# Optimization experiments

Measured on AMD Instinct MI355X. Metric: run time of the kernel, lower is better.

## Reference

```python
import jax, jax.numpy as jnp
import numpy as np

HIDDEN = 2048
HEAD = 256
VDIM = 512  # double_v_dim=True -> 2*head_size
GAMMA = 0.96875
SCALE_BASE = 512.0  # xpos default


def _rotate_every_two(x):
    # (x0, x1, x2, x3, ...) -> (-x1, x0, -x3, x2, ...)
    x1 = x[..., ::2]
    x2 = x[..., 1::2]
    return jnp.stack((-x2, x1), axis=-1).reshape(x.shape)


def _xpos(x, downscale=False, offset=0):
    # Standard XPOS (rotary + exponential scaling) as used in RetNet repos.
    S, d = x.shape[1], x.shape[2]
    d2 = d // 2
    scale_vec = (jnp.arange(0, d, 2, dtype=jnp.float32) + 0.4 * d) / (1.4 * d)  # [d2]
    pos = jnp.arange(S + offset, dtype=jnp.float32)
    scale = scale_vec[None, :] ** (pos[:, None] / SCALE_BASE)  # [S+off, d2]
    inv_freq = 1.0 / (10000.0 ** (jnp.arange(d2, dtype=jnp.float32) / d2))
    sinusoid = pos[:, None] * inv_freq[None, :]  # [S+off, d2]
    sin, cos = jnp.sin(sinusoid), jnp.cos(sinusoid)
    scale, sin, cos = scale[-S:], sin[-S:], cos[-S:]
    if downscale:
        scale = 1.0 / scale
    sin_s = jnp.repeat(sin * scale, 2, axis=-1)  # duplicate_interleave -> [S, d]
    cos_s = jnp.repeat(cos * scale, 2, axis=-1)
    return x * cos_s[None] + _rotate_every_two(x) * sin_s[None]


def _decay_matrix(S):
    # D[n, m] = gamma^(n-m) for n >= m else 0 (NaN/overflow-safe)
    n = jnp.arange(S, dtype=jnp.float32)
    diff = n[:, None] - n[None, :]
    mask = diff >= 0
    return jnp.where(mask, GAMMA ** jnp.where(mask, diff, 0.0), 0.0)


def setup_inputs() -> dict:
    key = jax.random.key(0)
    k1, k2, k3, k4 = jax.random.split(key, 4)
    B, S = 4, 4096
    X = jax.random.normal(k1, (B, S, HIDDEN), dtype=jnp.float32)
    W_Q = jax.random.normal(k2, (HIDDEN, HEAD), dtype=jnp.float32) / HIDDEN
    W_K = jax.random.normal(k3, (HIDDEN, HEAD), dtype=jnp.float32) / HIDDEN
    W_V = jax.random.normal(k4, (HIDDEN, VDIM), dtype=jnp.float32) / HIDDEN
    return {"X": X, "W_Q": W_Q, "W_K": W_K, "W_V": W_V}


def reference(X, W_Q, W_K, W_V):
    S = X.shape[1]
    Q = _xpos(X @ W_Q)                      # [B, S, HEAD]
    K = _xpos(X @ W_K, downscale=True)      # [B, S, HEAD]
    V = X @ W_V                             # [B, S, VDIM]
    D = _decay_matrix(S)                    # [S, S]
    retention = jnp.einsum('bqd,bkd->bqk', Q, K) * D[None]  # [B, S, S]
    return retention @ V                    # [B, S, VDIM]
```

## Files before the change

### kernel.cpp

```cpp
#include <hip/hip_runtime.h>
#include <math.h>

#define NB 4
#define SEQ 4096
#define HID 2048
#define DH 256
#define DV 512
#define NQKV 1024
#define CHUNK 128
#define NCH 32
#define MROWS (NB * SEQ)
#define GAMMA 0.96875f
#define GAMMA_INV 1.0322580645161290f
#define LOG2_GAMMA (-0.045803689613124794f)
#define LOG2_10000 13.287712379549449f

typedef __attribute__((ext_vector_type(8))) short short8;
typedef __attribute__((ext_vector_type(4))) float floatx4;

__device__ __forceinline__ unsigned short bf16_rne(float v) {
    unsigned int u = __float_as_uint(v);
    u += 0x7fff + ((u >> 16) & 1);
    return (unsigned short)(u >> 16);
}
__device__ __forceinline__ float b2f(unsigned short h) {
    return __uint_as_float((unsigned int)h << 16);
}

__device__ __forceinline__ void gld16(const void* g, void* l) {
    __builtin_amdgcn_global_load_lds(
        reinterpret_cast<const __attribute__((address_space(1))) unsigned int*>(
            reinterpret_cast<uintptr_t>(g)),
        reinterpret_cast<__attribute__((address_space(3))) unsigned int*>(
            reinterpret_cast<uintptr_t>(l)),
        16, 0, 0);
}

__global__ __launch_bounds__(256) void xcvt_kernel(
    const float* __restrict__ X, unsigned short* __restrict__ Xb)
{
    const int i = blockIdx.x * 256 + threadIdx.x;
    float4 x = ((const float4*)X)[i];
    ushort4 h;
    h.x = bf16_rne(x.x); h.y = bf16_rne(x.y);
    h.z = bf16_rne(x.z); h.w = bf16_rne(x.w);
    ((ushort4*)Xb)[i] = h;
}

__global__ __launch_bounds__(256) void wcvt_kernel(
    const float* __restrict__ WQ, const float* __restrict__ WK,
    const float* __restrict__ WV, unsigned short* __restrict__ Bt)
{
    __shared__ unsigned short sh[64][65];
    const int bid = blockIdx.x;
    const int kt = bid & 31;
    const int ntile = bid >> 5;
    const int k0 = kt * 64, n0 = ntile * 64;

    const float* W; int ld, nl0;
    if (n0 < 256)      { W = WQ; ld = DH; nl0 = n0; }
    else if (n0 < 512) { W = WK; ld = DH; nl0 = n0 - 256; }
    else               { W = WV; ld = DV; nl0 = n0 - 512; }

    const int t = threadIdx.x;
#pragma unroll
    for (int p = 0; p < 4; p++) {
        const int kl = (t >> 4) + p * 16;
        const int ng = (t & 15) * 4;
        float4 w = *(const float4*)&W[(size_t)(k0 + kl) * ld + nl0 + ng];
        sh[kl][ng + 0] = bf16_rne(w.x);
        sh[kl][ng + 1] = bf16_rne(w.y);
        sh[kl][ng + 2] = bf16_rne(w.z);
        sh[kl][ng + 3] = bf16_rne(w.w);
    }
    __syncthreads();
#pragma unroll
    for (int p = 0; p < 4; p++) {
        const int nl = (t >> 4) + p * 16;
        const int kg = (t & 15) * 4;
        ushort4 h;
        h.x = sh[kg + 0][nl]; h.y = sh[kg + 1][nl];
        h.z = sh[kg + 2][nl]; h.w = sh[kg + 3][nl];
        *(ushort4*)&Bt[(size_t)(n0 + nl) * HID + k0 + kg] = h;
    }
}

__global__ __launch_bounds__(256, 2) void qkv_mfma_kernel(
    const unsigned short* __restrict__ Xb, const unsigned short* __restrict__ Bt,
    unsigned short* __restrict__ Qb, unsigned short* __restrict__ Kb,
    unsigned short* __restrict__ Kt, unsigned short* __restrict__ Vt)
{
    __shared__ unsigned short Ah[2 * 128 * 32];
    __shared__ unsigned short Bh[2 * 128 * 32];

    const int bid = blockIdx.x;
    const int xcd = bid & 7;
    const int nt  = (bid >> 3) & 7;
    const int mt  = (xcd << 4) | (bid >> 6);
    const int m0 = mt * 128, n0 = nt * 128;

    const int t = threadIdx.x;
    const int w = t >> 6, lane = t & 63;
    const int wm = (w & 1) << 6;
    const int wn = (w >> 1) << 6;

    floatx4 acc[4][4];
#pragma unroll
    for (int i = 0; i < 4; i++)
#pragma unroll
        for (int j = 0; j < 4; j++) acc[i][j] = (floatx4)0.0f;

    const int srow = lane >> 2, scol = (lane & 3) * 8;
    const size_t aoff = (size_t)(m0 + w * 32 + srow) * HID + scol;
    const size_t boff = (size_t)(n0 + w * 32 + srow) * HID + scol;

    const int fr = lane & 15, fq = (lane >> 4) * 8;

    for (int k0 = 0; k0 < HID; k0 += 64) {
        __syncthreads();
#pragma unroll
        for (int s = 0; s < 2; s++)
#pragma unroll
            for (int q = 0; q < 2; q++) {
                gld16(Xb + aoff + (size_t)q * 16 * HID + k0 + s * 32,
                      &Ah[s * 4096 + (w * 32 + q * 16) * 32]);
                gld16(Bt + boff + (size_t)q * 16 * HID + k0 + s * 32,
                      &Bh[s * 4096 + (w * 32 + q * 16) * 32]);
            }
        __syncthreads();

#pragma nounroll
        for (int s = 0; s < 2; s++) {
            short8 ah[4], bh[4];
#pragma unroll
            for (int i = 0; i < 4; i++)
                ah[i] = *(const short8*)&Ah[s * 4096 + (wm + i * 16 + fr) * 32 + fq];
#pragma unroll
            for (int j = 0; j < 4; j++)
                bh[j] = *(const short8*)&Bh[s * 4096 + (wn + j * 16 + fr) * 32 + fq];
#pragma unroll
            for (int i = 0; i < 4; i++)
#pragma unroll
                for (int j = 0; j < 4; j++)
                    acc[i][j] = __builtin_amdgcn_mfma_f32_16x16x32_bf16(ah[i], bh[j], acc[i][j], 0, 0, 0);
        }
    }

    const int cl = lane & 15, rq = (lane >> 4) << 2;
    if (n0 >= 512) {
#pragma unroll
        for (int i = 0; i < 4; i++)
#pragma unroll
            for (int j = 0; j < 4; j++) {
                const int c = n0 - 512 + wn + j * 16 + cl;
#pragma unroll
                for (int r = 0; r < 4; r++) {
                    const int m = m0 + wm + i * 16 + rq + r;
                    Vt[(size_t)c * MROWS + m] = bf16_rne(acc[i][j][r]);
                }
            }
    } else {
        const bool isQ = (n0 < 256);
        unsigned short* dst = isQ ? Qb : Kb;
        const float sgn = isQ ? 1.f : -1.f;
        const int nb = isQ ? n0 : n0 - 256;
#pragma unroll
        for (int j = 0; j < 4; j++) {
            const int c = nb + wn + j * 16 + cl;
            const float jj = (float)(c >> 1);
            const float sv = (2.f * jj + 0.4f * 256.f) * (1.f / (1.4f * 256.f));
            const float l2sv = __log2f(sv) * sgn * (1.f / 512.f);
            const float invf = exp2f(jj * (-LOG2_10000 / 128.f));
            const bool odd = (c & 1) != 0;
#pragma unroll
            for (int i = 0; i < 4; i++) {
#pragma unroll
                for (int r = 0; r < 4; r++) {
                    const int m = m0 + wm + i * 16 + rq + r;
                    const float s = (float)(m & (SEQ - 1));
                    const float x = acc[i][j][r];
                    const float p = __shfl_xor(x, 1, 64);
                    const float sc = exp2f(s * l2sv);
                    const float ang = s * invf;
                    const float sn = __sinf(ang), cs = __cosf(ang);
                    const float o = odd ? sc * (x * cs + p * sn)
                                        : sc * (x * cs - p * sn);
                    const unsigned short hv = bf16_rne(o);
                    dst[(size_t)m * DH + c] = hv;
                    if (!isQ) Kt[(size_t)c * MROWS + m] = hv;
                }
            }
        }
    }
}

__global__ __launch_bounds__(512, 1) void chunk_kv_kernel(
    const unsigned short* __restrict__ Kt, const unsigned short* __restrict__ Vt,
    float* __restrict__ Ut)
{
    __shared__ unsigned short As[128 * 32];
    __shared__ unsigned short Bs[128 * 32];

    const int bid = blockIdx.x;
    const int dht = bid & 1;
    const int vq  = (bid >> 1) & 3;
    const int c   = (bid >> 3) & 31;
    const int b   = bid >> 8;
    const int dh0 = dht * 128, dv0 = vq * 128;
    const int row0 = b * SEQ + c * CHUNK;

    const int t = threadIdx.x;
    const int w = t >> 6, lane = t & 63;
    const int wm = (w & 1) << 6;
    const int wn = (w >> 1) << 5;
    const int srow = lane >> 2, scol = (lane & 3) * 8;
    const int fr = lane & 15, fq = (lane >> 4) * 8;

    floatx4 acc[4][2];
#pragma unroll
    for (int i = 0; i < 4; i++)
#pragma unroll
        for (int j = 0; j < 2; j++) acc[i][j] = (floatx4)0.0f;

    const int kr = t >> 2, kc = (t & 3) * 8;

    for (int i0 = 0; i0 < CHUNK; i0 += 32) {
        __syncthreads();
        gld16(&Vt[(size_t)(dv0 + w * 16 + srow) * MROWS + row0 + i0 + scol],
              &As[(w * 16) * 32]);
        {
            const unsigned short* src = &Kt[(size_t)(dh0 + kr) * MROWS + row0 + i0 + kc];
            ushort4 k0v = *(const ushort4*)src;
            ushort4 k1v = *(const ushort4*)(src + 4);
            float g = exp2f((float)(CHUNK - i0 - kc) * LOG2_GAMMA);
            ushort4 h0, h1;
            h0.x = bf16_rne(b2f(k0v.x) * g); g *= GAMMA_INV;
            h0.y = bf16_rne(b2f(k0v.y) * g); g *= GAMMA_INV;
            h0.z = bf16_rne(b2f(k0v.z) * g); g *= GAMMA_INV;
            h0.w = bf16_rne(b2f(k0v.w) * g); g *= GAMMA_INV;
            h1.x = bf16_rne(b2f(k1v.x) * g); g *= GAMMA_INV;
            h1.y = bf16_rne(b2f(k1v.y) * g); g *= GAMMA_INV;
            h1.z = bf16_rne(b2f(k1v.z) * g); g *= GAMMA_INV;
            h1.w = bf16_rne(b2f(k1v.w) * g);
            *(ushort4*)&Bs[kr * 32 + kc] = h0;
            *(ushort4*)&Bs[kr * 32 + kc + 4] = h1;
        }
        __syncthreads();
        short8 a[4], bb[2];
#pragma unroll
        for (int i = 0; i < 4; i++)
            a[i] = *(const short8*)&As[(wm + i * 16 + fr) * 32 + fq];
#pragma unroll
        for (int j = 0; j < 2; j++)
            bb[j] = *(const short8*)&Bs[(wn + j * 16 + fr) * 32 + fq];
#pragma unroll
        for (int i = 0; i < 4; i++)
#pragma unroll
            for (int j = 0; j < 2; j++)
                acc[i][j] = __builtin_amdgcn_mfma_f32_16x16x32_bf16(a[i], bb[j], acc[i][j], 0, 0, 0);
    }

    const int cl = lane & 15, rq = (lane >> 4) << 2;
    const size_t ubase = ((size_t)(b * NCH + c) * DV + dv0) * DH + dh0;
#pragma unroll
    for (int i = 0; i < 4; i++)
#pragma unroll
        for (int j = 0; j < 2; j++) {
            const int n = wn + j * 16 + cl;
#pragma unroll
            for (int r = 0; r < 4; r++) {
                const int m = wm + i * 16 + rq + r;
                Ut[ubase + (size_t)m * DH + n] = acc[i][j][r];
            }
        }
}

__global__ __launch_bounds__(256) void scan_kernel(
    const float* __restrict__ Ut, unsigned short* __restrict__ Sb)
{
    const int t = blockIdx.x * 256 + threadIdx.x;
    const int b = t >> 17;
    const int r = t & 131071;
    const float gC = exp2f((float)CHUNK * LOG2_GAMMA);
    float s = 0.f;
    const size_t base = (size_t)b * NCH * 131072 + r;
    for (int c = 0; c < NCH; c++) {
        const size_t off = base + (size_t)c * 131072;
        const float u = Ut[off];
        Sb[off] = bf16_rne(s);
        s = gC * s + u;
    }
}

__global__ __launch_bounds__(512, 1) void out_mfma_kernel(
    const unsigned short* __restrict__ Qb, const unsigned short* __restrict__ Kb,
    const unsigned short* __restrict__ Vt, const unsigned short* __restrict__ Sb,
    float* __restrict__ out)
{
    __shared__ unsigned short Pa[128 * 136];
    __shared__ unsigned short As[2 * 128 * 32];
    __shared__ unsigned short Bs[2 * 128 * 32];

    const int bid = blockIdx.x;
    const int vq = bid & 3;
    const int c  = (bid >> 2) & 31;
    const int b  = bid >> 7;
    const int dv0 = vq * 128;
    const int row0 = b * SEQ + c * CHUNK;

    const int t = threadIdx.x;
    const int w = t >> 6, lane = t & 63;
    const int wm = (w & 1) << 6;
    const int wn = (w >> 1) << 5;
    const int fr = lane & 15, fq = (lane >> 4) * 8;
    const int cl = lane & 15, rq = (lane >> 4) << 2;
    const int srow = lane >> 2, scol = (lane & 3) * 8;

    floatx4 acc[4][2];
#pragma unroll
    for (int i = 0; i < 4; i++)
#pragma unroll
        for (int j = 0; j < 2; j++) acc[i][j] = (floatx4)0.0f;

    for (int d0 = 0; d0 < DH; d0 += 64) {
        __syncthreads();
        gld16(&Qb[(size_t)(row0 + w * 16 + srow) * DH + d0 + scol], &As[(w * 16) * 32]);
        gld16(&Qb[(size_t)(row0 + w * 16 + srow) * DH + d0 + 32 + scol], &As[4096 + (w * 16) * 32]);
        gld16(&Kb[(size_t)(row0 + w * 16 + srow) * DH + d0 + scol], &Bs[(w * 16) * 32]);
        gld16(&Kb[(size_t)(row0 + w * 16 + srow) * DH + d0 + 32 + scol], &Bs[4096 + (w * 16) * 32]);
        __syncthreads();
#pragma nounroll
        for (int s = 0; s < 2; s++) {
            short8 a[4], bb[2];
#pragma unroll
            for (int i = 0; i < 4; i++)
                a[i] = *(const short8*)&As[s * 4096 + (wm + i * 16 + fr) * 32 + fq];
#pragma unroll
            for (int j = 0; j < 2; j++)
                bb[j] = *(const short8*)&Bs[s * 4096 + (wn + j * 16 + fr) * 32 + fq];
#pragma unroll
            for (int i = 0; i < 4; i++)
#pragma unroll
                for (int j = 0; j < 2; j++)
                    acc[i][j] = __builtin_amdgcn_mfma_f32_16x16x32_bf16(a[i], bb[j], acc[i][j], 0, 0, 0);
        }
    }

#pragma unroll
    for (int i = 0; i < 4; i++)
#pragma unroll
        for (int j = 0; j < 2; j++) {
            const int jj = wn + j * 16 + cl;
#pragma unroll
            for (int r = 0; r < 4; r++) {
                const int ii = wm + i * 16 + rq + r;
                const int diff = ii - jj;
                const float v = (diff >= 0) ? acc[i][j][r] * exp2f((float)diff * LOG2_GAMMA) : 0.f;
                Pa[ii * 136 + jj] = bf16_rne(v);
            }
            acc[i][j] = (floatx4)0.0f;
        }

    for (int k0 = 0; k0 < CHUNK; k0 += 64) {
        __syncthreads();
        gld16(&Vt[(size_t)(dv0 + w * 16 + srow) * MROWS + row0 + k0 + scol], &Bs[(w * 16) * 32]);
        gld16(&Vt[(size_t)(dv0 + w * 16 + srow) * MROWS + row0 + k0 + 32 + scol], &Bs[4096 + (w * 16) * 32]);
        __syncthreads();
#pragma nounroll
        for (int s = 0; s < 2; s++) {
            short8 a[4], bb[2];
#pragma unroll
            for (int i = 0; i < 4; i++)
                a[i] = *(const short8*)&Pa[(wm + i * 16 + fr) * 136 + k0 + s * 32 + fq];
#pragma unroll
            for (int j = 0; j < 2; j++)
                bb[j] = *(const short8*)&Bs[s * 4096 + (wn + j * 16 + fr) * 32 + fq];
#pragma unroll
            for (int i = 0; i < 4; i++)
#pragma unroll
                for (int j = 0; j < 2; j++)
                    acc[i][j] = __builtin_amdgcn_mfma_f32_16x16x32_bf16(a[i], bb[j], acc[i][j], 0, 0, 0);
        }
    }

    const size_t sbbase = ((size_t)(b * NCH + c) * DV + dv0) * DH;
    const int xr = t >> 2, xc = (t & 3) * 8;
    const float gx = exp2f((float)xr * LOG2_GAMMA);
    for (int d0 = 0; d0 < DH; d0 += 64) {
        __syncthreads();
#pragma unroll
        for (int s = 0; s < 2; s++) {
            const unsigned short* src = &Qb[(size_t)(row0 + xr) * DH + d0 + s * 32 + xc];
            ushort4 q0 = *(const ushort4*)src;
            ushort4 q1 = *(const ushort4*)(src + 4);
            ushort4 h0, h1;
            h0.x = bf16_rne(b2f(q0.x) * gx); h0.y = bf16_rne(b2f(q0.y) * gx);
            h0.z = bf16_rne(b2f(q0.z) * gx); h0.w = bf16_rne(b2f(q0.w) * gx);
            h1.x = bf16_rne(b2f(q1.x) * gx); h1.y = bf16_rne(b2f(q1.y) * gx);
            h1.z = bf16_rne(b2f(q1.z) * gx); h1.w = bf16_rne(b2f(q1.w) * gx);
            *(ushort4*)&As[s * 4096 + xr * 32 + xc] = h0;
            *(ushort4*)&As[s * 4096 + xr * 32 + xc + 4] = h1;
        }
        gld16(&Sb[sbbase + (size_t)(w * 16 + srow) * DH + d0 + scol], &Bs[(w * 16) * 32]);
        gld16(&Sb[sbbase + (size_t)(w * 16 + srow) * DH + d0 + 32 + scol], &Bs[4096 + (w * 16) * 32]);
        __syncthreads();
#pragma nounroll
        for (int s = 0; s < 2; s++) {
            short8 a[4], bb[2];
#pragma unroll
            for (int i = 0; i < 4; i++)
                a[i] = *(const short8*)&As[s * 4096 + (wm + i * 16 + fr) * 32 + fq];
#pragma unroll
            for (int j = 0; j < 2; j++)
                bb[j] = *(const short8*)&Bs[s * 4096 + (wn + j * 16 + fr) * 32 + fq];
#pragma unroll
            for (int i = 0; i < 4; i++)
#pragma unroll
                for (int j = 0; j < 2; j++)
                    acc[i][j] = __builtin_amdgcn_mfma_f32_16x16x32_bf16(a[i], bb[j], acc[i][j], 0, 0, 0);
        }
    }

#pragma unroll
    for (int i = 0; i < 4; i++)
#pragma unroll
        for (int j = 0; j < 2; j++) {
            const int dv = dv0 + wn + j * 16 + cl;
#pragma unroll
            for (int r = 0; r < 4; r++) {
                const int m = row0 + wm + i * 16 + rq + r;
                out[(size_t)m * DV + dv] = acc[i][j][r];
            }
        }
}

extern "C" void kernel_launch(void* const* d_in, const int* in_sizes, int n_in,
                              void* d_out, int out_size, void* d_ws, size_t ws_size,
                              hipStream_t stream) {
    const float* X  = (const float*)d_in[0];
    const float* WQ = (const float*)d_in[1];
    const float* WK = (const float*)d_in[2];
    const float* WV = (const float*)d_in[3];
    float* out = (float*)d_out;

    char* ws = (char*)d_ws;
    unsigned short* Qb = (unsigned short*)ws;
    unsigned short* Kb = Qb + (size_t)MROWS * DH;
    unsigned short* Kt = Kb + (size_t)MROWS * DH;
    unsigned short* Vt = Kt + (size_t)MROWS * DH;
    unsigned short* Sb = Vt + (size_t)MROWS * DV;
    float*          Ut = (float*)(Sb + (size_t)NB * NCH * DV * DH);
    unsigned short* Xb = (unsigned short*)Ut;
    unsigned short* Bt = (unsigned short*)(Ut + (size_t)NB * NCH * DV * DH);

    xcvt_kernel<<<(MROWS * HID / 4) / 256, 256, 0, stream>>>(X, Xb);
    wcvt_kernel<<<512, 256, 0, stream>>>(WQ, WK, WV, Bt);
    qkv_mfma_kernel<<<1024, 256, 0, stream>>>(Xb, Bt, Qb, Kb, Kt, Vt);
    chunk_kv_kernel<<<1024, 512, 0, stream>>>(Kt, Vt, Ut);
    scan_kernel<<<2048, 256, 0, stream>>>(Ut, Sb);
    out_mfma_kernel<<<512, 512, 0, stream>>>(Qb, Kb, Vt, Sb, out);
}
```

Before: 371.7 us.

## Double-buffer QKV GEMM shared tiles with XOR-swizzled layout

Rewrites the QKV projection GEMM main loop to use two shared-memory buffers per operand. The global-to-LDS loads for the next 64-wide K slice are issued while MFMAs run on the current slice, which removes one barrier per iteration. It also stores rows as 64-element lines with an XOR swizzle on the 16-byte segment index, meant to avoid LDS bank conflicts on the fragment reads. Shared memory per block doubles to 64 KB, which may limit occupancy against the launch bound of 2 blocks per CU.

```diff
diff --git a/kernel.cpp b/kernel.cpp
--- a/kernel.cpp
+++ b/kernel.cpp
@@ -90,8 +90,10 @@
     unsigned short* __restrict__ Qb, unsigned short* __restrict__ Kb,
     unsigned short* __restrict__ Kt, unsigned short* __restrict__ Vt)
 {
-    __shared__ unsigned short Ah[2 * 128 * 32];
-    __shared__ unsigned short Bh[2 * 128 * 32];
+    __shared__ unsigned short A0[128 * 64];
+    __shared__ unsigned short A1[128 * 64];
+    __shared__ unsigned short B0[128 * 64];
+    __shared__ unsigned short B1[128 * 64];
 
     const int bid = blockIdx.x;
     const int xcd = bid & 7;
@@ -110,40 +112,54 @@
 #pragma unroll
         for (int j = 0; j < 4; j++) acc[i][j] = (floatx4)0.0f;
 
-    const int srow = lane >> 2, scol = (lane & 3) * 8;
-    const size_t aoff = (size_t)(m0 + w * 32 + srow) * HID + scol;
-    const size_t boff = (size_t)(n0 + w * 32 + srow) * HID + scol;
-
-    const int fr = lane & 15, fq = (lane >> 4) * 8;
-
-    for (int k0 = 0; k0 < HID; k0 += 64) {
-        __syncthreads();
-#pragma unroll
-        for (int s = 0; s < 2; s++)
-#pragma unroll
-            for (int q = 0; q < 2; q++) {
-                gld16(Xb + aoff + (size_t)q * 16 * HID + k0 + s * 32,
-                      &Ah[s * 4096 + (w * 32 + q * 16) * 32]);
-                gld16(Bt + boff + (size_t)q * 16 * HID + k0 + s * 32,
-                      &Bh[s * 4096 + (w * 32 + q * 16) * 32]);
-            }
-        __syncthreads();
-
-#pragma nounroll
-        for (int s = 0; s < 2; s++) {
-            short8 ah[4], bh[4];
-#pragma unroll
-            for (int i = 0; i < 4; i++)
-                ah[i] = *(const short8*)&Ah[s * 4096 + (wm + i * 16 + fr) * 32 + fq];
-#pragma unroll
-            for (int j = 0; j < 4; j++)
-                bh[j] = *(const short8*)&Bh[s * 4096 + (wn + j * 16 + fr) * 32 + fq];
-#pragma unroll
-            for (int i = 0; i < 4; i++)
-#pragma unroll
-                for (int j = 0; j < 4; j++)
-                    acc[i][j] = __builtin_amdgcn_mfma_f32_16x16x32_bf16(ah[i], bh[j], acc[i][j], 0, 0, 0);
-        }
+    const int rl = lane >> 3;
+    const int sg = (lane & 7) ^ rl;
+    const unsigned short* const gA = Xb + (size_t)(m0 + w * 32 + rl) * HID + sg * 8;
+    const unsigned short* const gB = Bt + (size_t)(n0 + w * 32 + rl) * HID + sg * 8;
+
+#define QKV_STAGE(Adst, Bdst, kk)                                             \
+    {                                                                         \
+        _Pragma("unroll")                                                     \
+        for (int q = 0; q < 4; q++) {                                         \
+            gld16(gA + (size_t)q * 8 * HID + (kk), &Adst[(w * 32 + q * 8) * 64]); \
+            gld16(gB + (size_t)q * 8 * HID + (kk), &Bdst[(w * 32 + q * 8) * 64]); \
+        }                                                                     \
+    }
+
+    const int fr = lane & 15;
+    const int g  = lane >> 4;
+    const int x7 = fr & 7;
+
+#define QKV_COMPUTE(Abuf, Bbuf)                                               \
+    {                                                                         \
+        _Pragma("nounroll")                                                   \
+        for (int h = 0; h < 2; h++) {                                         \
+            const int soff = ((((h << 2) | g) ^ x7) << 3);                    \
+            short8 ah[4], bh[4];                                              \
+            _Pragma("unroll")                                                 \
+            for (int i = 0; i < 4; i++)                                       \
+                ah[i] = *(const short8*)&Abuf[(wm + i * 16 + fr) * 64 + soff];\
+            _Pragma("unroll")                                                 \
+            for (int j = 0; j < 4; j++)                                       \
+                bh[j] = *(const short8*)&Bbuf[(wn + j * 16 + fr) * 64 + soff];\
+            _Pragma("unroll")                                                 \
+            for (int i = 0; i < 4; i++)                                       \
+                _Pragma("unroll")                                             \
+                for (int j = 0; j < 4; j++)                                   \
+                    acc[i][j] = __builtin_amdgcn_mfma_f32_16x16x32_bf16(      \
+                        ah[i], bh[j], acc[i][j], 0, 0, 0);                    \
+        }                                                                     \
+    }
+
+    QKV_STAGE(A0, B0, 0);
+    __syncthreads();
+    for (int k0 = 0; k0 < HID; k0 += 128) {
+        QKV_STAGE(A1, B1, k0 + 64);
+        QKV_COMPUTE(A0, B0);
+        __syncthreads();
+        if (k0 + 128 < HID) QKV_STAGE(A0, B0, k0 + 128);
+        QKV_COMPUTE(A1, B1);
+        __syncthreads();
     }
 
     const int cl = lane & 15, rq = (lane >> 4) << 2;
```

Measured after the change: 361.8 us. -2.7%, faster.

## Use 256x256 double-buffered swizzled-LDS tiles in QKV projection GEMM

Applied to the files above, without the earlier changes.

The QKV projection GEMM moves from 128x128 tiles with 4 waves to 256x256 tiles with 8 waves, each holding a 128x64 accumulator block. Global-to-LDS loads are now double-buffered so the next K tile is fetched while MFMAs run on the current one. An XOR swizzle on LDS columns avoids bank conflicts, and barriers plus setprio interleave LDS reads with MFMA phases. This cuts global traffic per FLOP and hides load latency, at the cost of higher register and LDS pressure and only 256 blocks, which may underfill the GPU.

```diff
diff --git a/kernel.cpp b/kernel.cpp
--- a/kernel.cpp
+++ b/kernel.cpp
@@ -6,7 +6,6 @@
 #define HID 2048
 #define DH 256
 #define DV 512
-#define NQKV 1024
 #define CHUNK 128
 #define NCH 32
 #define MROWS (NB * SEQ)
@@ -85,77 +84,144 @@
     }
 }
 
-__global__ __launch_bounds__(256, 2) void qkv_mfma_kernel(
+__global__ __launch_bounds__(512, 2) void qkv_mfma_kernel(
     const unsigned short* __restrict__ Xb, const unsigned short* __restrict__ Bt,
     unsigned short* __restrict__ Qb, unsigned short* __restrict__ Kb,
     unsigned short* __restrict__ Kt, unsigned short* __restrict__ Vt)
 {
-    __shared__ unsigned short Ah[2 * 128 * 32];
-    __shared__ unsigned short Bh[2 * 128 * 32];
+    __shared__ unsigned short lds[2 * 32768];
 
     const int bid = blockIdx.x;
     const int xcd = bid & 7;
-    const int nt  = (bid >> 3) & 7;
-    const int mt  = (xcd << 4) | (bid >> 6);
-    const int m0 = mt * 128, n0 = nt * 128;
+    const int idx = bid >> 3;
+    const int mt  = (xcd << 3) | (idx >> 2);
+    const int nt  = idx & 3;
+    const int m0 = mt * 256, n0 = nt * 256;
 
     const int t = threadIdx.x;
     const int w = t >> 6, lane = t & 63;
-    const int wm = (w & 1) << 6;
-    const int wn = (w >> 1) << 6;
-
-    floatx4 acc[4][4];
-#pragma unroll
-    for (int i = 0; i < 4; i++)
+    const int wr = w >> 2;
+    const int wc = w & 3;
+
+    floatx4 acc[8][4];
+#pragma unroll
+    for (int i = 0; i < 8; i++)
 #pragma unroll
         for (int j = 0; j < 4; j++) acc[i][j] = (floatx4)0.0f;
 
-    const int srow = lane >> 2, scol = (lane & 3) * 8;
-    const size_t aoff = (size_t)(m0 + w * 32 + srow) * HID + scol;
-    const size_t boff = (size_t)(n0 + w * 32 + srow) * HID + scol;
-
-    const int fr = lane & 15, fq = (lane >> 4) * 8;
-
-    for (int k0 = 0; k0 < HID; k0 += 64) {
-        __syncthreads();
-#pragma unroll
-        for (int s = 0; s < 2; s++)
-#pragma unroll
-            for (int q = 0; q < 2; q++) {
-                gld16(Xb + aoff + (size_t)q * 16 * HID + k0 + s * 32,
-                      &Ah[s * 4096 + (w * 32 + q * 16) * 32]);
-                gld16(Bt + boff + (size_t)q * 16 * HID + k0 + s * 32,
-                      &Bh[s * 4096 + (w * 32 + q * 16) * 32]);
-            }
-        __syncthreads();
-
-#pragma nounroll
-        for (int s = 0; s < 2; s++) {
-            short8 ah[4], bh[4];
-#pragma unroll
-            for (int i = 0; i < 4; i++)
-                ah[i] = *(const short8*)&Ah[s * 4096 + (wm + i * 16 + fr) * 32 + fq];
-#pragma unroll
-            for (int j = 0; j < 4; j++)
-                bh[j] = *(const short8*)&Bh[s * 4096 + (wn + j * 16 + fr) * 32 + fq];
-#pragma unroll
-            for (int i = 0; i < 4; i++)
-#pragma unroll
-                for (int j = 0; j < 4; j++)
-                    acc[i][j] = __builtin_amdgcn_mfma_f32_16x16x32_bf16(ah[i], bh[j], acc[i][j], 0, 0, 0);
-        }
-    }
+    const int rl = lane >> 3;
+    const int sg = (lane & 7) ^ rl;
+
+    const int fr = lane & 15, g = lane >> 4;
+    const int x7 = fr & 7;
+    const int soff0 = ((g ^ x7) << 3);
+    const int soff1 = (((4 | g) ^ x7) << 3);
+
+#define STAGE_HT(isB, h, dbuf, kt)                                            \
+    {                                                                         \
+        const unsigned short* gsrc =                                          \
+            ((isB) ? Bt + (size_t)(n0 + (h) * 128 + w * 16 + rl) * HID        \
+                   : Xb + (size_t)(m0 + (h) * 128 + w * 16 + rl) * HID)       \
+            + (size_t)(kt) * 64 + sg * 8;                                     \
+        unsigned short* ldst = &lds[(dbuf) * 32768 + ((isB) ? 16384 : 0)      \
+                                    + ((h) * 128 + w * 16) * 64];             \
+        gld16(gsrc, ldst);                                                    \
+        gld16(gsrc + (size_t)8 * HID, ldst + 8 * 64);                         \
+    }
+
+#define READ_A(ih)                                                            \
+    _Pragma("unroll")                                                         \
+    for (int i2 = 0; i2 < 4; i2++) {                                          \
+        const int row = wr * 128 + ((ih) * 4 + i2) * 16 + fr;                 \
+        ah[i2][0] = *(const short8*)&lds[cb + row * 64 + soff0];              \
+        ah[i2][1] = *(const short8*)&lds[cb + row * 64 + soff1];              \
+    }
+
+#define READ_B(jh)                                                            \
+    _Pragma("unroll")                                                         \
+    for (int j2 = 0; j2 < 2; j2++) {                                          \
+        const int row = wc * 64 + ((jh) * 2 + j2) * 16 + fr;                  \
+        bh[(jh) * 2 + j2][0] = *(const short8*)&lds[cb + 16384 + row * 64 + soff0]; \
+        bh[(jh) * 2 + j2][1] = *(const short8*)&lds[cb + 16384 + row * 64 + soff1]; \
+    }
+
+#define MFMA16(ib, jb)                                                        \
+    _Pragma("unroll")                                                         \
+    for (int i2 = 0; i2 < 4; i2++)                                            \
+        _Pragma("unroll")                                                     \
+        for (int j2 = 0; j2 < 2; j2++) {                                      \
+            acc[(ib) + i2][(jb) + j2] = __builtin_amdgcn_mfma_f32_16x16x32_bf16( \
+                ah[i2][0], bh[(jb) + j2][0], acc[(ib) + i2][(jb) + j2], 0, 0, 0); \
+            acc[(ib) + i2][(jb) + j2] = __builtin_amdgcn_mfma_f32_16x16x32_bf16( \
+                ah[i2][1], bh[(jb) + j2][1], acc[(ib) + i2][(jb) + j2], 0, 0, 0); \
+        }
+
+    STAGE_HT(0, 0, 0, 0); STAGE_HT(0, 1, 0, 0);
+    STAGE_HT(1, 0, 0, 0); STAGE_HT(1, 1, 0, 0);
+    asm volatile("s_waitcnt vmcnt(0)" ::: "memory");
+    __builtin_amdgcn_s_barrier();
+    __builtin_amdgcn_sched_barrier(0);
+
+    int cur = 0;
+    for (int kt = 0; kt < 32; ++kt) {
+        const int nxt = cur ^ 1;
+        if (kt + 1 < 32) {
+            STAGE_HT(0, 0, nxt, kt + 1); STAGE_HT(0, 1, nxt, kt + 1);
+            STAGE_HT(1, 0, nxt, kt + 1); STAGE_HT(1, 1, nxt, kt + 1);
+        }
+        const int cb = cur * 32768;
+        short8 ah[4][2], bh[4][2];
+
+        READ_A(0); READ_B(0);
+        __builtin_amdgcn_s_barrier();
+        __builtin_amdgcn_sched_barrier(0);
+        __builtin_amdgcn_s_setprio(1);
+        MFMA16(0, 0);
+        __builtin_amdgcn_s_setprio(0);
+        __builtin_amdgcn_s_barrier();
+        __builtin_amdgcn_sched_barrier(0);
+
+        READ_B(1);
+        __builtin_amdgcn_s_barrier();
+        __builtin_amdgcn_sched_barrier(0);
+        __builtin_amdgcn_s_setprio(1);
+        MFMA16(0, 2);
+        __builtin_amdgcn_s_setprio(0);
+        __builtin_amdgcn_s_barrier();
+        __builtin_amdgcn_sched_barrier(0);
+
+        READ_A(1);
+        __builtin_amdgcn_s_barrier();
+        __builtin_amdgcn_sched_barrier(0);
+        __builtin_amdgcn_s_setprio(1);
+        MFMA16(4, 0);
+        __builtin_amdgcn_s_setprio(0);
+        __builtin_amdgcn_s_barrier();
+        __builtin_amdgcn_sched_barrier(0);
+
+        __builtin_amdgcn_s_setprio(1);
+        MFMA16(4, 2);
+        __builtin_amdgcn_s_setprio(0);
+        asm volatile("s_waitcnt vmcnt(0)" ::: "memory");
+        __builtin_amdgcn_s_barrier();
+        __builtin_amdgcn_sched_barrier(0);
+        cur = nxt;
+    }
+#undef STAGE_HT
+#undef READ_A
+#undef READ_B
+#undef MFMA16
 
     const int cl = lane & 15, rq = (lane >> 4) << 2;
     if (n0 >= 512) {
 #pragma unroll
-        for (int i = 0; i < 4; i++)
+        for (int i = 0; i < 8; i++)
 #pragma unroll
             for (int j = 0; j < 4; j++) {
-                const int c = n0 - 512 + wn + j * 16 + cl;
+                const int c = n0 - 512 + wc * 64 + j * 16 + cl;
 #pragma unroll
                 for (int r = 0; r < 4; r++) {
-                    const int m = m0 + wm + i * 16 + rq + r;
+                    const int m = m0 + wr * 128 + i * 16 + rq + r;
                     Vt[(size_t)c * MROWS + m] = bf16_rne(acc[i][j][r]);
                 }
             }
@@ -163,20 +229,19 @@
         const bool isQ = (n0 < 256);
         unsigned short* dst = isQ ? Qb : Kb;
         const float sgn = isQ ? 1.f : -1.f;
-        const int nb = isQ ? n0 : n0 - 256;
 #pragma unroll
         for (int j = 0; j < 4; j++) {
-            const int c = nb + wn + j * 16 + cl;
+            const int c = wc * 64 + j * 16 + cl;
             const float jj = (float)(c >> 1);
             const float sv = (2.f * jj + 0.4f * 256.f) * (1.f / (1.4f * 256.f));
             const float l2sv = __log2f(sv) * sgn * (1.f / 512.f);
             const float invf = exp2f(jj * (-LOG2_10000 / 128.f));
             const bool odd = (c & 1) != 0;
 #pragma unroll
-            for (int i = 0; i < 4; i++) {
+            for (int i = 0; i < 8; i++) {
 #pragma unroll
                 for (int r = 0; r < 4; r++) {
-                    const int m = m0 + wm + i * 16 + rq + r;
+                    const int m = m0 + wr * 128 + i * 16 + rq + r;
                     const float s = (float)(m & (SEQ - 1));
                     const float x = acc[i][j][r];
                     const float p = __shfl_xor(x, 1, 64);
@@ -455,7 +520,7 @@
 
     xcvt_kernel<<<(MROWS * HID / 4) / 256, 256, 0, stream>>>(X, Xb);
     wcvt_kernel<<<512, 256, 0, stream>>>(WQ, WK, WV, Bt);
-    qkv_mfma_kernel<<<1024, 256, 0, stream>>>(Xb, Bt, Qb, Kb, Kt, Vt);
+    qkv_mfma_kernel<<<256, 512, 0, stream>>>(Xb, Bt, Qb, Kb, Kt, Vt);
     chunk_kv_kernel<<<1024, 512, 0, stream>>>(Kt, Vt, Ut);
     scan_kernel<<<2048, 256, 0, stream>>>(Ut, Sb);
     out_mfma_kernel<<<512, 512, 0, stream>>>(Qb, Kb, Vt, Sb, out);
```

Measured after the change: 367.7 us. No clear change (-1.1%).
